# Kernel optimization log

Hardware: AMD Instinct MI355X
Metric: run time of the kernel (lower is better)

## Reference

```python
import jax, jax.numpy as jnp
import numpy as np

NUM_HEADS = 16
D_MODEL = 1024
BATCH = 8
SEQ = 1024


def setup_inputs() -> dict:
    key = jax.random.key(0)
    ks = jax.random.split(key, 8)
    inv = 1.0 / np.sqrt(D_MODEL)
    return {
        "query": jax.random.normal(ks[0], (BATCH, SEQ, D_MODEL), dtype=jnp.float32),
        "key": jax.random.normal(ks[1], (BATCH, SEQ, D_MODEL), dtype=jnp.float32),
        "value": jax.random.normal(ks[2], (BATCH, SEQ, D_MODEL), dtype=jnp.float32),
        "mask": jax.random.randint(ks[3], (BATCH, SEQ), 0, 2, dtype=jnp.int32),
        "Wq": jax.random.normal(ks[4], (D_MODEL, D_MODEL), dtype=jnp.float32) * inv,
        "bq": jax.random.normal(ks[5], (D_MODEL,), dtype=jnp.float32) * inv,
        "Wo": jax.random.normal(ks[6], (D_MODEL, D_MODEL), dtype=jnp.float32) * inv,
        "bo": jax.random.normal(ks[7], (D_MODEL,), dtype=jnp.float32) * inv,
    }


def reference(query, key, value, mask, Wq, bq, Wo, bo):
    b, s, d = query.shape
    H = NUM_HEADS
    dk = d // H
    # NOTE: the original torch module (faithfully reproduced) applies
    # query_project to query, key AND value; key/value projections are dead.
    def proj(x):
        return (x @ Wq.T + bq).reshape(b, s, H, dk).transpose(0, 2, 1, 3)  # (b,H,s,dk)

    q, k, v = proj(query), proj(key), proj(value)

    m = mask.astype(query.dtype)                       # (b,s)
    score_mask = (m[:, :, None] * m[:, None, :])[:, None]  # (b,1,s,s), broadcasts over heads

    scale = 1.0 / jnp.sqrt(jnp.asarray(dk, dtype=query.dtype))
    score = jnp.einsum("bhqd,bhkd->bhqk", q, k) * scale  # (b,H,s,s)
    score = jnp.where(score_mask == 0, jnp.asarray(-1e9, dtype=score.dtype), score)
    # softmax then post-softmax mask multiply (the non-standard double-masking)
    p_attn = jax.nn.softmax(score, axis=-1) * score_mask  # (b,H,s,s)

    x = jnp.einsum("bhqk,bhkd->bhqd", p_attn, v)  # (b,H,s,dk)
    x = x.transpose(0, 2, 1, 3).reshape(b, s, d)
    out = x @ Wo.T + bo
    return out, p_attn
```

## Files before the change

kernel.cpp:

```cpp
#include <hip/hip_runtime.h>
#include <cstddef>
#include <cstdint>

#define BATCH   8
#define SEQ     1024
#define DMODEL  1024
#define NHEADS  16
#define DKH     64
#define NE      (BATCH*SEQ*DMODEL)
#define WE      (DMODEL*DMODEL)
#define NE4     (NE/4)
#define WE4     (WE/4)

typedef __attribute__((ext_vector_type(8))) short bf16x8;
typedef __attribute__((ext_vector_type(4))) short s16x4;
typedef __attribute__((ext_vector_type(4))) float f32x4;

#define MFMA16(a,b,c) __builtin_amdgcn_mfma_f32_16x16x32_bf16(a,b,c,0,0,0)

__device__ __forceinline__ unsigned short f2bf(float f) {
    uint32_t u = __float_as_uint(f);
    u += 0x7fffu + ((u >> 16) & 1u);
    return (unsigned short)(u >> 16);
}
__device__ __forceinline__ float bf2f(unsigned short s) {
    return __uint_as_float(((uint32_t)s) << 16);
}

__device__ __forceinline__ void gload16(const void* g, void* l) {
    __builtin_amdgcn_global_load_lds(
        (const __attribute__((address_space(1))) void*)g,
        (__attribute__((address_space(3))) void*)l, 16, 0, 0);
}

__global__ void cvt_all(const float* __restrict__ q, const float* __restrict__ k,
                        const float* __restrict__ v, const float* __restrict__ wq,
                        const float* __restrict__ wo,
                        unsigned short* __restrict__ qkv, unsigned short* __restrict__ wqh,
                        unsigned short* __restrict__ woh)
{
    const int i = blockIdx.x * blockDim.x + threadIdx.x;
    const float* src; unsigned short* dst; int j;
    if (i < 3 * NE4) {
        const int seg = i >> 21;
        j = i & (NE4 - 1);
        src = (seg == 0) ? q : ((seg == 1) ? k : v);
        dst = qkv + (size_t)seg * NE;
    } else {
        const int i2 = i - 3 * NE4;
        if (i2 < WE4) { j = i2; src = wq; dst = wqh; }
        else          { j = i2 - WE4; src = wo; dst = woh; }
    }
    const f32x4 x = ((const f32x4*)src)[j];
    s16x4 h4;
    #pragma unroll
    for (int e = 0; e < 4; ++e) h4[e] = (short)f2bf(x[e]);
    ((s16x4*)dst)[j] = h4;
}

#define GBM 128
#define GBN 128
#define GBK 32

template<int OUTMODE>
__global__ __launch_bounds__(256, 2)
void gemm_mfma(const unsigned short* __restrict__ Ab,
               const unsigned short* __restrict__ Whi, const float* __restrict__ bias,
               unsigned short* __restrict__ Ohi, unsigned short* __restrict__ Ovt,
               float* __restrict__ Of)
{
    __shared__ unsigned short sT[2][2][GBM * GBK];

    const int tid = threadIdx.x, lane = tid & 63, wid = tid >> 6;
    const int m0 = blockIdx.y * GBM, n0 = blockIdx.x * GBN;
    const int wm = (wid >> 1) * 64, wn = (wid & 1) * 64;
    const int lo = lane & 15, hi4 = lane >> 4;

    const int gs = (lane & 3) ^ ((lane >> 3) & 3);
    const size_t arow0 = (size_t)(m0 + wid * 32 + (lane >> 2));
    const size_t wrow0 = (size_t)(n0 + wid * 32 + (lane >> 2));
    const unsigned short* aSrc0 = &Ab[arow0 * DMODEL + gs * 8];
    const unsigned short* aSrc1 = &Ab[(arow0 + 16) * DMODEL + gs * 8];
    const unsigned short* wSrc0 = &Whi[wrow0 * DMODEL + gs * 8];
    const unsigned short* wSrc1 = &Whi[(wrow0 + 16) * DMODEL + gs * 8];

    f32x4 acc[4][4] = {};

    {
        unsigned short* dA = &sT[0][0][(wid * 2) * 512];
        unsigned short* dW = &sT[0][1][(wid * 2) * 512];
        gload16(aSrc0, dA);       gload16(aSrc1, dA + 512);
        gload16(wSrc0, dW);       gload16(wSrc1, dW + 512);
    }

    for (int kt = 0; kt < DMODEL / GBK; ++kt) {
        __syncthreads();
        if (kt + 1 < DMODEL / GBK) {
            const int kn = (kt + 1) * GBK;
            unsigned short* dA = &sT[(kt + 1) & 1][0][(wid * 2) * 512];
            unsigned short* dW = &sT[(kt + 1) & 1][1][(wid * 2) * 512];
            gload16(aSrc0 + kn, dA);   gload16(aSrc1 + kn, dA + 512);
            gload16(wSrc0 + kn, dW);   gload16(wSrc1 + kn, dW + 512);
        }
        const unsigned short* aB = &sT[kt & 1][0][0];
        const unsigned short* wB = &sT[kt & 1][1][0];
        const int swz = (hi4 ^ ((lo >> 1) & 3)) * 8;
        bf16x8 ah[4], bh_[4];
        #pragma unroll
        for (int m = 0; m < 4; ++m)
            ah[m] = *(const bf16x8*)&aB[(wm + m * 16 + lo) * GBK + swz];
        #pragma unroll
        for (int n = 0; n < 4; ++n)
            bh_[n] = *(const bf16x8*)&wB[(wn + n * 16 + lo) * GBK + swz];
        #pragma unroll
        for (int m = 0; m < 4; ++m)
            #pragma unroll
            for (int n = 0; n < 4; ++n)
                acc[m][n] = MFMA16(ah[m], bh_[n], acc[m][n]);
    }

    const int seg = m0 >> 13;
    #pragma unroll
    for (int n = 0; n < 4; ++n) {
        const int col = n0 + wn + n * 16 + lo;
        const float bv = bias[col];
        #pragma unroll
        for (int m = 0; m < 4; ++m) {
            if (OUTMODE == 3 && seg == 2) {
                const int row0 = (m0 + wm + m * 16 + hi4 * 4) & 8191;
                const int b = row0 >> 10, s0_ = row0 & 1023;
                const int h = col >> 6, di = col & 63;
                s16x4 o;
                #pragma unroll
                for (int j = 0; j < 4; ++j) o[j] = (short)f2bf(acc[m][n][j] + bv);
                *(s16x4*)&Ovt[(((size_t)(b * NHEADS + h)) * DKH + di) * SEQ + s0_] = o;
            } else {
                #pragma unroll
                for (int j = 0; j < 4; ++j) {
                    const int row = m0 + wm + m * 16 + hi4 * 4 + j;
                    const float f = acc[m][n][j] + bv;
                    if (OUTMODE == 3) {
                        const int rs = row & 8191;
                        const int b = rs >> 10, s = rs & 1023;
                        const int h = col >> 6, di = col & 63;
                        unsigned short* dst = Ohi + (size_t)seg * NE;
                        dst[(((size_t)(b * NHEADS + h)) * SEQ + s) * DKH + di] = f2bf(f);
                    } else {
                        Of[(size_t)row * DMODEL + col] = f;
                    }
                }
            }
        }
    }
}

#define ALD 72

__global__ __launch_bounds__(512, 4)
void attn_fused(const unsigned short* __restrict__ qhi, const unsigned short* __restrict__ khi,
                const unsigned short* __restrict__ vt, const int* __restrict__ mask,
                float* __restrict__ pattn, unsigned short* __restrict__ xb)
{
    __shared__ unsigned short sQh[128 * ALD];
    __shared__ unsigned short sKh[64 * ALD];
    __shared__ unsigned short sVt[64 * ALD];
    __shared__ int sM[SEQ];
    __shared__ float sP32[8][16 * 68];

    const int blk = blockIdx.x;
    const int idx = blk >> 3;
    const int bh = (blk & 7) * 16 + (idx & 15);
    const int qt = idx >> 4;
    const int b = bh >> 4, h = bh & 15;
    const int q0 = qt * 128;
    const int tid = threadIdx.x, lane = tid & 63, wid = tid >> 6;
    const int lo = lane & 15, hi = lane >> 4;

    *(int2*)&sM[tid * 2] = *(const int2*)&mask[b * SEQ + tid * 2];
    #pragma unroll
    for (int c = 0; c < 2; ++c) {
        const int id = tid * 2 + c, row = id >> 3, col = (id & 7) * 8;
        *(bf16x8*)&sQh[row * ALD + col] =
            *(const bf16x8*)&qhi[((size_t)bh * SEQ + q0 + row) * DKH + col];
    }
    __syncthreads();

    const int qrow = wid * 16 + lo;
    bf16x8 aqh[2];
    aqh[0] = *(const bf16x8*)&sQh[qrow * ALD + hi * 8];
    aqh[1] = *(const bf16x8*)&sQh[qrow * ALD + 32 + hi * 8];
    int mqr[4];
    #pragma unroll
    for (int j = 0; j < 4; ++j) mqr[j] = sM[q0 + wid * 16 + hi * 4 + j];

    const int srow = tid >> 3, scol = (tid & 7) * 8;
    const unsigned short* kbase = &khi[(size_t)bh * SEQ * DKH + (size_t)srow * DKH + scol];
    const unsigned short* vbase = &vt[(size_t)bh * DKH * SEQ + (size_t)srow * SEQ + scol];

    float l4[4] = {0.f, 0.f, 0.f, 0.f};
    bf16x8 kr = *(const bf16x8*)kbase;
    for (int kt = 0; kt < 16; ++kt) {
        __syncthreads();
        *(bf16x8*)&sKh[srow * ALD + scol] = kr;
        __syncthreads();
        if (kt < 15) kr = *(const bf16x8*)(kbase + (size_t)(kt + 1) * 64 * DKH);
        f32x4 acc4[4] = {};
        #pragma unroll
        for (int ks = 0; ks < 2; ++ks)
            #pragma unroll
            for (int n = 0; n < 4; ++n)
                acc4[n] = MFMA16(aqh[ks],
                    *(const bf16x8*)&sKh[(n * 16 + lo) * ALD + ks * 32 + hi * 8], acc4[n]);
        #pragma unroll
        for (int n = 0; n < 4; ++n) {
            const int mkc = sM[kt * 64 + n * 16 + lo];
            #pragma unroll
            for (int j = 0; j < 4; ++j)
                l4[j] += (mqr[j] && mkc) ? __expf(acc4[n][j] * 0.125f) : 0.f;
        }
    }
    float rinv[4];
    #pragma unroll
    for (int j = 0; j < 4; ++j) {
        float s = l4[j];
        #pragma unroll
        for (int o = 1; o < 16; o <<= 1) s += __shfl_xor(s, o, 16);
        rinv[j] = (s > 0.f) ? (1.0f / s) : 0.f;
    }

    f32x4 oacc[4] = {};
    kr = *(const bf16x8*)kbase;
    bf16x8 vr = *(const bf16x8*)vbase;
    for (int kt = 0; kt < 16; ++kt) {
        __syncthreads();
        *(bf16x8*)&sKh[srow * ALD + scol] = kr;
        *(bf16x8*)&sVt[srow * ALD + scol] = vr;
        __syncthreads();
        if (kt < 15) {
            kr = *(const bf16x8*)(kbase + (size_t)(kt + 1) * 64 * DKH);
            vr = *(const bf16x8*)(vbase + (kt + 1) * 64);
        }
        f32x4 acc4[4] = {};
        #pragma unroll
        for (int ks = 0; ks < 2; ++ks)
            #pragma unroll
            for (int n = 0; n < 4; ++n)
                acc4[n] = MFMA16(aqh[ks],
                    *(const bf16x8*)&sKh[(n * 16 + lo) * ALD + ks * 32 + hi * 8], acc4[n]);

        #pragma unroll
        for (int n = 0; n < 4; ++n) {
            const int mkc = sM[kt * 64 + n * 16 + lo];
            #pragma unroll
            for (int j = 0; j < 4; ++j) {
                const float p = (mqr[j] && mkc) ? __expf(acc4[n][j] * 0.125f) * rinv[j] : 0.f;
                sP32[wid][(hi * 4 + j) * 68 + n * 16 + lo] = p;
            }
        }
        asm volatile("s_waitcnt lgkmcnt(0)" ::: "memory");
        __builtin_amdgcn_sched_barrier(0);

        #pragma unroll
        for (int rr = 0; rr < 4; ++rr) {
            const int prow = rr * 4 + hi;
            const f32x4 pv = *(const f32x4*)&sP32[wid][prow * 68 + lo * 4];
            *(f32x4*)&pattn[((size_t)bh * SEQ + q0 + wid * 16 + prow) * SEQ + kt * 64 + lo * 4] = pv;
        }
        #pragma unroll
        for (int ks = 0; ks < 2; ++ks) {
            const float* pp = &sP32[wid][lo * 68 + ks * 32 + hi * 8];
            const f32x4 p0 = *(const f32x4*)pp;
            const f32x4 p1 = *(const f32x4*)(pp + 4);
            bf16x8 ap;
            #pragma unroll
            for (int e = 0; e < 4; ++e) { ap[e] = (short)f2bf(p0[e]); ap[4 + e] = (short)f2bf(p1[e]); }
            #pragma unroll
            for (int n = 0; n < 4; ++n)
                oacc[n] = MFMA16(ap,
                    *(const bf16x8*)&sVt[(n * 16 + lo) * ALD + ks * 32 + hi * 8], oacc[n]);
        }
    }

    #pragma unroll
    for (int n = 0; n < 4; ++n)
        #pragma unroll
        for (int j = 0; j < 4; ++j) {
            const int row = q0 + wid * 16 + hi * 4 + j;
            const int col = h * DKH + n * 16 + lo;
            xb[(size_t)(b * SEQ + row) * DMODEL + col] = f2bf(oacc[n][j]);
        }
}

extern "C" void kernel_launch(void* const* d_in, const int* in_sizes, int n_in,
                              void* d_out, int out_size, void* d_ws, size_t ws_size,
                              hipStream_t stream) {
    (void)in_sizes; (void)n_in; (void)out_size; (void)ws_size;

    const float* query = (const float*)d_in[0];
    const float* key   = (const float*)d_in[1];
    const float* value = (const float*)d_in[2];
    const int*   mask  = (const int*)d_in[3];
    const float* Wq    = (const float*)d_in[4];
    const float* bq    = (const float*)d_in[5];
    const float* Wo    = (const float*)d_in[6];
    const float* bo    = (const float*)d_in[7];

    float* out   = (float*)d_out;
    float* pattn = out + (size_t)NE;

    char* w = (char*)d_ws;
    unsigned short* wqhi = (unsigned short*)w;  w += (size_t)WE * 2;
    unsigned short* wohi = (unsigned short*)w;  w += (size_t)WE * 2;
    unsigned short* qkv  = (unsigned short*)w;  w += (size_t)NE * 3 * 2;
    unsigned short* qhi  = (unsigned short*)w;  w += (size_t)NE * 2;
    unsigned short* khi  = (unsigned short*)w;  w += (size_t)NE * 2;
    unsigned short* vt   = (unsigned short*)w;  w += (size_t)NE * 2;
    unsigned short* xb   = (unsigned short*)w;  w += (size_t)NE * 2;
    (void)khi;

    cvt_all<<<(3 * NE4 + 2 * WE4) / 256, 256, 0, stream>>>(
        query, key, value, Wq, Wo, qkv, wqhi, wohi);

    gemm_mfma<3><<<dim3(DMODEL / GBN, 3 * (BATCH * SEQ) / GBM), 256, 0, stream>>>(
        qkv, wqhi, bq, qhi, vt, nullptr);

    attn_fused<<<BATCH * NHEADS * (SEQ / 128), 512, 0, stream>>>(qhi, khi, vt, mask, pattn, xb);

    gemm_mfma<2><<<dim3(DMODEL / GBN, (BATCH * SEQ) / GBM), 256, 0, stream>>>(
        xb, wohi, bo, nullptr, nullptr, out);
}
```

Measured before the change: 310.7 us.

## Fuse fp32-to-bf16 activation conversion into QKV projection GEMM and remap block order

Removes the separate conversion pass over query/key/value. The projection GEMM now loads fp32 activations into registers, converts them to bf16 and writes them into swizzled shared memory, with the conversion overlapped against the MFMA loop of the previous tile. The GEMM grid is flattened and remapped so blocks cycle through N tiles per XCD group, which aims at better L2 reuse. The p_attn output now uses nontemporal stores. This saves a full fp32 read and bf16 write/read round trip of the activations, at the cost of register-path loads and extra VALU work inside the GEMM.

```diff
diff --git a/kernel.cpp b/kernel.cpp
--- a/kernel.cpp
+++ b/kernel.cpp
@@ -9,7 +9,6 @@
 #define DKH     64
 #define NE      (BATCH*SEQ*DMODEL)
 #define WE      (DMODEL*DMODEL)
-#define NE4     (NE/4)
 #define WE4     (WE/4)
 
 typedef __attribute__((ext_vector_type(8))) short bf16x8;
@@ -33,24 +32,13 @@
         (__attribute__((address_space(3))) void*)l, 16, 0, 0);
 }
 
-__global__ void cvt_all(const float* __restrict__ q, const float* __restrict__ k,
-                        const float* __restrict__ v, const float* __restrict__ wq,
-                        const float* __restrict__ wo,
-                        unsigned short* __restrict__ qkv, unsigned short* __restrict__ wqh,
-                        unsigned short* __restrict__ woh)
+__global__ void cvt_w(const float* __restrict__ wq, const float* __restrict__ wo,
+                      unsigned short* __restrict__ wqh, unsigned short* __restrict__ woh)
 {
     const int i = blockIdx.x * blockDim.x + threadIdx.x;
     const float* src; unsigned short* dst; int j;
-    if (i < 3 * NE4) {
-        const int seg = i >> 21;
-        j = i & (NE4 - 1);
-        src = (seg == 0) ? q : ((seg == 1) ? k : v);
-        dst = qkv + (size_t)seg * NE;
-    } else {
-        const int i2 = i - 3 * NE4;
-        if (i2 < WE4) { j = i2; src = wq; dst = wqh; }
-        else          { j = i2 - WE4; src = wo; dst = woh; }
-    }
+    if (i < WE4) { src = wq; dst = wqh; j = i; }
+    else         { src = wo; dst = woh; j = i - WE4; }
     const f32x4 x = ((const f32x4*)src)[j];
     s16x4 h4;
     #pragma unroll
@@ -64,46 +52,80 @@
 
 template<int OUTMODE>
 __global__ __launch_bounds__(256, 2)
-void gemm_mfma(const unsigned short* __restrict__ Ab,
+void gemm_mfma(const float* __restrict__ Aq, const float* __restrict__ Ak,
+               const float* __restrict__ Av, const unsigned short* __restrict__ Ab,
                const unsigned short* __restrict__ Whi, const float* __restrict__ bias,
                unsigned short* __restrict__ Ohi, unsigned short* __restrict__ Ovt,
                float* __restrict__ Of)
 {
-    __shared__ unsigned short sT[2][2][GBM * GBK];
+    __shared__ unsigned short sA[2][GBM * GBK];
+    __shared__ unsigned short sW[2][GBM * GBK];
 
     const int tid = threadIdx.x, lane = tid & 63, wid = tid >> 6;
-    const int m0 = blockIdx.y * GBM, n0 = blockIdx.x * GBN;
+    const int cpx = gridDim.x >> 3;
+    const int L = (blockIdx.x & 7) * cpx + (blockIdx.x >> 3);
+    const int n0 = (L & 7) * GBN, m0 = (L >> 3) * GBM;
     const int wm = (wid >> 1) * 64, wn = (wid & 1) * 64;
     const int lo = lane & 15, hi4 = lane >> 4;
 
     const int gs = (lane & 3) ^ ((lane >> 3) & 3);
-    const size_t arow0 = (size_t)(m0 + wid * 32 + (lane >> 2));
     const size_t wrow0 = (size_t)(n0 + wid * 32 + (lane >> 2));
-    const unsigned short* aSrc0 = &Ab[arow0 * DMODEL + gs * 8];
-    const unsigned short* aSrc1 = &Ab[(arow0 + 16) * DMODEL + gs * 8];
     const unsigned short* wSrc0 = &Whi[wrow0 * DMODEL + gs * 8];
     const unsigned short* wSrc1 = &Whi[(wrow0 + 16) * DMODEL + gs * 8];
 
+    const int seg = (OUTMODE == 3) ? (m0 >> 13) : 0;
+    const float* Af = (OUTMODE == 3)
+        ? (seg == 0 ? Aq : (seg == 1 ? Ak : Av)) : nullptr;
+    const int mloc = m0 & 8191;
+    const int arow_s = (tid * 2) >> 2;
+    const int aslot0 = (tid * 2) & 3;
+    const int akey = (arow_s >> 1) & 3;
+    const float* aF0 = (OUTMODE == 3) ? &Af[(size_t)(mloc + arow_s) * DMODEL + (aslot0 ^ akey) * 8] : nullptr;
+    const float* aF1 = (OUTMODE == 3) ? &Af[(size_t)(mloc + arow_s) * DMODEL + ((aslot0 + 1) ^ akey) * 8] : nullptr;
+    const size_t arow0 = (size_t)(m0 + wid * 32 + (lane >> 2));
+    const unsigned short* aSrc0 = (OUTMODE == 2) ? &Ab[arow0 * DMODEL + gs * 8] : nullptr;
+    const unsigned short* aSrc1 = (OUTMODE == 2) ? &Ab[(arow0 + 16) * DMODEL + gs * 8] : nullptr;
+
     f32x4 acc[4][4] = {};
-
+    f32x4 ar0, ar1, ar2, ar3;
+
+    if (OUTMODE == 3) {
+        ar0 = *(const f32x4*)aF0; ar1 = *(const f32x4*)(aF0 + 4);
+        ar2 = *(const f32x4*)aF1; ar3 = *(const f32x4*)(aF1 + 4);
+        bf16x8 h0, h1;
+        #pragma unroll
+        for (int e = 0; e < 4; ++e) {
+            h0[e] = (short)f2bf(ar0[e]); h0[4 + e] = (short)f2bf(ar1[e]);
+            h1[e] = (short)f2bf(ar2[e]); h1[4 + e] = (short)f2bf(ar3[e]);
+        }
+        *(bf16x8*)&sA[0][arow_s * GBK + aslot0 * 8]       = h0;
+        *(bf16x8*)&sA[0][arow_s * GBK + (aslot0 + 1) * 8] = h1;
+    } else {
+        unsigned short* dA = &sA[0][(wid * 2) * 512];
+        gload16(aSrc0, dA);  gload16(aSrc1, dA + 512);
+    }
     {
-        unsigned short* dA = &sT[0][0][(wid * 2) * 512];
-        unsigned short* dW = &sT[0][1][(wid * 2) * 512];
-        gload16(aSrc0, dA);       gload16(aSrc1, dA + 512);
-        gload16(wSrc0, dW);       gload16(wSrc1, dW + 512);
+        unsigned short* dW = &sW[0][(wid * 2) * 512];
+        gload16(wSrc0, dW);  gload16(wSrc1, dW + 512);
     }
 
     for (int kt = 0; kt < DMODEL / GBK; ++kt) {
         __syncthreads();
+        const int nb = (kt + 1) & 1;
         if (kt + 1 < DMODEL / GBK) {
             const int kn = (kt + 1) * GBK;
-            unsigned short* dA = &sT[(kt + 1) & 1][0][(wid * 2) * 512];
-            unsigned short* dW = &sT[(kt + 1) & 1][1][(wid * 2) * 512];
-            gload16(aSrc0 + kn, dA);   gload16(aSrc1 + kn, dA + 512);
-            gload16(wSrc0 + kn, dW);   gload16(wSrc1 + kn, dW + 512);
-        }
-        const unsigned short* aB = &sT[kt & 1][0][0];
-        const unsigned short* wB = &sT[kt & 1][1][0];
+            if (OUTMODE == 3) {
+                ar0 = *(const f32x4*)(aF0 + kn); ar1 = *(const f32x4*)(aF0 + kn + 4);
+                ar2 = *(const f32x4*)(aF1 + kn); ar3 = *(const f32x4*)(aF1 + kn + 4);
+            } else {
+                unsigned short* dA = &sA[nb][(wid * 2) * 512];
+                gload16(aSrc0 + kn, dA);  gload16(aSrc1 + kn, dA + 512);
+            }
+            unsigned short* dW = &sW[nb][(wid * 2) * 512];
+            gload16(wSrc0 + kn, dW);  gload16(wSrc1 + kn, dW + 512);
+        }
+        const unsigned short* aB = &sA[kt & 1][0];
+        const unsigned short* wB = &sW[kt & 1][0];
         const int swz = (hi4 ^ ((lo >> 1) & 3)) * 8;
         bf16x8 ah[4], bh_[4];
         #pragma unroll
@@ -117,9 +139,19 @@
             #pragma unroll
             for (int n = 0; n < 4; ++n)
                 acc[m][n] = MFMA16(ah[m], bh_[n], acc[m][n]);
-    }
-
-    const int seg = m0 >> 13;
+
+        if (OUTMODE == 3 && kt + 1 < DMODEL / GBK) {
+            bf16x8 h0, h1;
+            #pragma unroll
+            for (int e = 0; e < 4; ++e) {
+                h0[e] = (short)f2bf(ar0[e]); h0[4 + e] = (short)f2bf(ar1[e]);
+                h1[e] = (short)f2bf(ar2[e]); h1[4 + e] = (short)f2bf(ar3[e]);
+            }
+            *(bf16x8*)&sA[nb][arow_s * GBK + aslot0 * 8]       = h0;
+            *(bf16x8*)&sA[nb][arow_s * GBK + (aslot0 + 1) * 8] = h1;
+        }
+    }
+
     #pragma unroll
     for (int n = 0; n < 4; ++n) {
         const int col = n0 + wn + n * 16 + lo;
@@ -264,7 +296,8 @@
         for (int rr = 0; rr < 4; ++rr) {
             const int prow = rr * 4 + hi;
             const f32x4 pv = *(const f32x4*)&sP32[wid][prow * 68 + lo * 4];
-            *(f32x4*)&pattn[((size_t)bh * SEQ + q0 + wid * 16 + prow) * SEQ + kt * 64 + lo * 4] = pv;
+            __builtin_nontemporal_store(pv,
+                (f32x4*)&pattn[((size_t)bh * SEQ + q0 + wid * 16 + prow) * SEQ + kt * 64 + lo * 4]);
         }
         #pragma unroll
         for (int ks = 0; ks < 2; ++ks) {
@@ -311,21 +344,18 @@
     char* w = (char*)d_ws;
     unsigned short* wqhi = (unsigned short*)w;  w += (size_t)WE * 2;
     unsigned short* wohi = (unsigned short*)w;  w += (size_t)WE * 2;
-    unsigned short* qkv  = (unsigned short*)w;  w += (size_t)NE * 3 * 2;
     unsigned short* qhi  = (unsigned short*)w;  w += (size_t)NE * 2;
     unsigned short* khi  = (unsigned short*)w;  w += (size_t)NE * 2;
     unsigned short* vt   = (unsigned short*)w;  w += (size_t)NE * 2;
     unsigned short* xb   = (unsigned short*)w;  w += (size_t)NE * 2;
-    (void)khi;
-
-    cvt_all<<<(3 * NE4 + 2 * WE4) / 256, 256, 0, stream>>>(
-        query, key, value, Wq, Wo, qkv, wqhi, wohi);
-
-    gemm_mfma<3><<<dim3(DMODEL / GBN, 3 * (BATCH * SEQ) / GBM), 256, 0, stream>>>(
-        qkv, wqhi, bq, qhi, vt, nullptr);
+
+    cvt_w<<<2 * WE4 / 256, 256, 0, stream>>>(Wq, Wo, wqhi, wohi);
+
+    gemm_mfma<3><<<8 * (3 * BATCH * SEQ) / GBM, 256, 0, stream>>>(
+        query, key, value, nullptr, wqhi, bq, qhi, vt, nullptr);
 
     attn_fused<<<BATCH * NHEADS * (SEQ / 128), 512, 0, stream>>>(qhi, khi, vt, mask, pattn, xb);
 
-    gemm_mfma<2><<<dim3(DMODEL / GBN, (BATCH * SEQ) / GBM), 256, 0, stream>>>(
-        xb, wohi, bo, nullptr, nullptr, out);
-}
+    gemm_mfma<2><<<8 * (BATCH * SEQ) / GBM, 256, 0, stream>>>(
+        nullptr, nullptr, nullptr, xb, wohi, bo, nullptr, nullptr, out);
+}
```

New measurement: 264.0 us. 15.0% less time.
